# Optimization experiments

Measured on AMD Instinct MI355X. Metric: run time of the kernel, lower is better.

The kernel has to match this reference:

```python
import jax, jax.numpy as jnp
import numpy as np

B, S, D, H = 2, 2048, 1024, 16
DH = D // H
SCALE = 1.0 / np.sqrt(D).astype(np.float32)  # module uses sqrt(d_model), not sqrt(d_h)


def setup_inputs() -> dict:
    key = jax.random.key(0)
    ks = jax.random.split(key, 11)
    def lin(k):
        kw, kb = jax.random.split(k)
        W = jax.random.normal(kw, (D, D), jnp.float32) * 0.02
        b = jax.random.normal(kb, (D,), jnp.float32) * 0.02
        return W, b
    Wq, bq = lin(ks[0]); Wk, bk = lin(ks[1]); Wv, bv = lin(ks[2]); Wo, bo = lin(ks[3])
    Q = jax.random.normal(ks[4], (B, S, D), jnp.float32)
    K = jax.random.normal(ks[5], (B, S, D), jnp.float32)
    V = jax.random.normal(ks[6], (B, S, D), jnp.float32)
    mask = jnp.triu(jnp.ones((S, S), jnp.bool_), k=1)  # True = masked (causal)
    return {"Q": Q, "K": K, "V": V, "mask": mask,
            "Wq": Wq, "bq": bq, "Wk": Wk, "bk": bk,
            "Wv": Wv, "bv": bv, "Wo": Wo, "bo": bo}


def reference(Q, K, V, mask, Wq, bq, Wk, bk, Wv, bv, Wo, bo):
    # Linear projections (torch Linear: x @ W^T + b; W here stored pre-transposed)
    q = Q @ Wq + bq  # [B,S,D]
    k = K @ Wk + bk
    v = V @ Wv + bv
    # Faithful (scrambled) head split: transpose then reshape for Q and K
    qh = jnp.transpose(q, (0, 2, 1)).reshape(B, H, S, DH)
    kh = jnp.transpose(jnp.transpose(k, (0, 2, 1)).reshape(B, H, S, DH), (0, 1, 3, 2))  # [B,H,DH,S]
    score = jax.nn.softmax(jnp.matmul(qh, kh) * SCALE, axis=-1)  # [B,H,S,S]
    # Faithful post-softmax masking
    score = jnp.where(mask, jnp.float32(-1e9), score)
    # V is reshaped directly (no transpose) per the source
    att = jnp.matmul(score, v.reshape(B, H, S, DH))  # [B,H,S,DH]
    att = att.reshape(B, S, D)
    return att @ Wo + bo  # dropout is identity in eval
```

## Files before the change

### kernel.cpp

```cpp
#include <hip/hip_runtime.h>
#include <hip/hip_bf16.h>


typedef __hip_bfloat16 bf16;
typedef __attribute__((ext_vector_type(8))) short bf16x8;
typedef __attribute__((ext_vector_type(4))) float f32x4;
typedef __attribute__((address_space(1))) const unsigned int guint;
typedef __attribute__((address_space(3))) unsigned int luint;

constexpr size_t OFF_WCUMT  = 0;
constexpr size_t OFF_WBIGT  = 524288;
constexpr size_t OFF_VB     = 1572864;
constexpr size_t OFF_WVB    = 3670016;
constexpr size_t OFF_UBIG   = 4194304;
constexpr size_t OFF_WOSUMT = 8388608;
constexpr size_t OFF_WVFT   = 8454144;
constexpr size_t OFF_BBIG   = 8519680;
constexpr size_t OFF_BVF    = 8521728;
constexpr size_t OFF_FLAG   = 8521792;

__device__ __forceinline__ float toF(bf16 x)  { return __bfloat162float(x); }
__device__ __forceinline__ float toF(float x) { return x; }
__device__ __forceinline__ unsigned short f2b_bits(float f) {
    unsigned u = __float_as_uint(f);
    return (unsigned short)((u + 0x7FFF + ((u >> 16) & 1)) >> 16);
}

__global__ __launch_bounds__(256) void detect_dtype(const unsigned short* __restrict__ Vraw,
                                                    int* __restrict__ flag) {
    __shared__ int cnt[256];
    const int t = threadIdx.x;
    int weird = 0;
    #pragma unroll
    for (int j = 0; j < 8; ++j) {
        unsigned short h = Vraw[2 * (t * 8 + j)];
        int e = (h >> 7) & 0xFF;
        bool w = (e >= 127 + 21) || (e != 0 && e <= 127 - 21) ||
                 (e == 0 && (h & 0x7F));
        weird += w ? 1 : 0;
    }
    cnt[t] = weird;
    __syncthreads();
    #pragma unroll
    for (int s = 128; s > 0; s >>= 1) {
        if (t < s) cnt[t] += cnt[t + s];
        __syncthreads();
    }
    if (t == 0) *flag = (cnt[0] < 512) ? 1 : 0;
}

__global__ __launch_bounds__(256) void conv_f2b(const float* __restrict__ V,
                                                const float* __restrict__ Wv,
                                                bf16* __restrict__ Vb,
                                                bf16* __restrict__ Wvb,
                                                const int* __restrict__ flag) {
    if (*flag != 0) return;
    int i = blockIdx.x * 256 + threadIdx.x;
    float4 v;
    ushort4* dst;
    if (i < 1048576) {
        v = ((const float4*)V)[i];
        dst = ((ushort4*)Vb) + i;
    } else {
        int j = i - 1048576;
        if (j >= 262144) return;
        v = ((const float4*)Wv)[j];
        dst = ((ushort4*)Wvb) + j;
    }
    ushort4 h;
    h.x = f2b_bits(v.x); h.y = f2b_bits(v.y);
    h.z = f2b_bits(v.z); h.w = f2b_bits(v.w);
    *dst = h;
}

__global__ __launch_bounds__(256) void fold_weights(const void* __restrict__ WoR,
                                                    const void* __restrict__ WvR,
                                                    const void* __restrict__ bvR,
                                                    bf16* __restrict__ WcumT,
                                                    float* __restrict__ WoSumT,
                                                    float* __restrict__ WvFT,
                                                    float* __restrict__ bvF,
                                                    const int* __restrict__ flag) {
    const int f = *flag;
    int idx = blockIdx.x * 256 + threadIdx.x;
    int a = idx >> 6, dh = idx & 63;
    float acc = 0.f;
    if (f == 1) {
        const bf16* Wo = (const bf16*)WoR;
        #pragma unroll
        for (int q = 0; q < 16; ++q) {
            WcumT[(size_t)a * 1024 + q * 64 + dh] = __float2bfloat16(acc);
            acc += toF(Wo[(size_t)(q * 64 + dh) * 1024 + a]);
        }
    } else {
        const float* Wo = (const float*)WoR;
        #pragma unroll
        for (int q = 0; q < 16; ++q) {
            WcumT[(size_t)a * 1024 + q * 64 + dh] = __float2bfloat16(acc);
            acc += Wo[(size_t)(q * 64 + dh) * 1024 + a];
        }
    }
    WoSumT[(size_t)a * 64 + dh] = acc;
    float acc2 = 0.f;
    if (f == 1) {
        const bf16* Wv = (const bf16*)WvR;
        #pragma unroll
        for (int q = 0; q < 16; ++q)
            acc2 += toF(Wv[(size_t)a * 1024 + q * 64 + dh]);
    } else {
        const float* Wv = (const float*)WvR;
        #pragma unroll
        for (int q = 0; q < 16; ++q)
            acc2 += Wv[(size_t)a * 1024 + q * 64 + dh];
    }
    WvFT[(size_t)dh * 1024 + a] = acc2;
    if (idx < 64) {
        float b = 0.f;
        if (f == 1) {
            const bf16* bv = (const bf16*)bvR;
            #pragma unroll
            for (int q = 0; q < 16; ++q) b += toF(bv[q * 64 + idx]);
        } else {
            const float* bv = (const float*)bvR;
            #pragma unroll
            for (int q = 0; q < 16; ++q) b += ((const float*)bvR)[q * 64 + idx];
        }
        bvF[idx] = b;
    }
}

__global__ __launch_bounds__(64) void reduce_bias(const void* __restrict__ bvR,
                                                  const bf16* __restrict__ WcumT,
                                                  const float* __restrict__ WoSumT,
                                                  const float* __restrict__ bvF,
                                                  float* __restrict__ bbig,
                                                  const int* __restrict__ flag) {
    const int f = *flag;
    const int n = blockIdx.x, t = threadIdx.x;
    float acc = 0.f;
    if (n < 1024) {
        if (f == 1) {
            const bf16* bv = (const bf16*)bvR;
            for (int d = t; d < 1024; d += 64)
                acc += toF(bv[d]) * toF(WcumT[(size_t)n * 1024 + d]);
        } else {
            const float* bv = (const float*)bvR;
            for (int d = t; d < 1024; d += 64)
                acc += bv[d] * toF(WcumT[(size_t)n * 1024 + d]);
        }
    } else {
        acc = bvF[t] * WoSumT[(size_t)(n - 1024) * 64 + t];
    }
    #pragma unroll
    for (int off = 32; off > 0; off >>= 1) acc += __shfl_down(acc, off);
    if (t == 0) bbig[n] = acc;
}

__global__ __launch_bounds__(256, 2)
void gemm128w2(const float* __restrict__ A, int lda,
               const float* __restrict__ Bm, int ldb,
               bf16* __restrict__ C, int ldc, int K) {
    __shared__ __align__(16) float As[16][128];
    __shared__ __align__(16) float Bs[16][128];
    const int tid = threadIdx.x;
    const int tx = tid & 15, ty = tid >> 4;
    const int gx = gridDim.x;
    int lin = blockIdx.y * gx + blockIdx.x;
    const int nwg = gx * gridDim.y;
    if ((nwg & 7) == 0) { const int per = nwg >> 3; lin = (lin & 7) * per + (lin >> 3); }
    const int m0 = (lin / gx) * 128;
    const int n0 = (lin % gx) * 128;
    const int arow = tid >> 1, ahalf = (tid & 1) * 8;
    const int brow = tid >> 4, bcol = (tid & 15) * 4;
    float acc[8][8] = {};
    for (int k0 = 0; k0 < K; k0 += 16) {
        {
            const float* ap = A + (size_t)(m0 + arow) * lda + (k0 + ahalf);
            float4 a0 = *(const float4*)ap, a1 = *(const float4*)(ap + 4);
            As[ahalf + 0][arow] = a0.x; As[ahalf + 1][arow] = a0.y;
            As[ahalf + 2][arow] = a0.z; As[ahalf + 3][arow] = a0.w;
            As[ahalf + 4][arow] = a1.x; As[ahalf + 5][arow] = a1.y;
            As[ahalf + 6][arow] = a1.z; As[ahalf + 7][arow] = a1.w;
        }
        {
            const float* bp = Bm + (size_t)(k0 + brow) * ldb + n0 + bcol;
            float4 b0 = *(const float4*)bp;
            float4 b1 = *(const float4*)(bp + 64);
            *(float4*)&Bs[brow][bcol]      = b0;
            *(float4*)&Bs[brow][bcol + 64] = b1;
        }
        __syncthreads();
        #pragma unroll
        for (int kk = 0; kk < 16; ++kk) {
            float4 aL = *(const float4*)&As[kk][ty * 4];
            float4 aH = *(const float4*)&As[kk][64 + ty * 4];
            float4 bL = *(const float4*)&Bs[kk][tx * 4];
            float4 bH = *(const float4*)&Bs[kk][64 + tx * 4];
            float a[8] = {aL.x, aL.y, aL.z, aL.w, aH.x, aH.y, aH.z, aH.w};
            float b[8] = {bL.x, bL.y, bL.z, bL.w, bH.x, bH.y, bH.z, bH.w};
            #pragma unroll
            for (int i = 0; i < 8; ++i)
                #pragma unroll
                for (int j = 0; j < 8; ++j)
                    acc[i][j] += a[i] * b[j];
        }
        __syncthreads();
    }
    #pragma unroll
    for (int ih = 0; ih < 2; ++ih)
        #pragma unroll
        for (int ii = 0; ii < 4; ++ii) {
            const int m = m0 + ih * 64 + ty * 4 + ii;
            bf16* crow = C + (size_t)m * ldc + n0;
            #pragma unroll
            for (int jh = 0; jh < 2; ++jh)
                #pragma unroll
                for (int j = 0; j < 4; ++j)
                    crow[jh * 64 + tx * 4 + j] =
                        __float2bfloat16(acc[ih * 4 + ii][jh * 4 + j]);
        }
}

__global__ __launch_bounds__(256, 2)
void mfma_nt(const bf16* __restrict__ Abf, const bf16* __restrict__ Aalt,
             const bf16* __restrict__ Bbf, const bf16* __restrict__ Balt,
             int lda, int ldb,
             const float* __restrict__ bias,
             bf16* __restrict__ C, int ldc, int K,
             const int* __restrict__ flag) {
    const bf16* A  = (*flag == 1) ? Abf : Aalt;
    const bf16* BT = (*flag == 1) ? Bbf : Balt;
    __shared__ __align__(16) short AsS[8192];
    __shared__ __align__(16) short BsS[8192];

    const int tid  = threadIdx.x;
    const int lane = tid & 63;
    const int w    = tid >> 6;
    const int wr   = w >> 1, wc = w & 1;

    const int gx = gridDim.x;
    int lin = blockIdx.y * gx + blockIdx.x;
    const int nwg = gx * gridDim.y;
    if ((nwg & 7) == 0) { const int per = nwg >> 3; lin = (lin & 7) * per + (lin >> 3); }
    const int m0 = (lin / gx) * 128;
    const int n0 = (lin % gx) * 128;

    const int srow = lane >> 3;
    const int sk   = 8 * ((lane & 7) ^ srow);
    const bf16* Ag = A  + (size_t)(m0 + w * 32 + srow) * lda + sk;
    const bf16* Bg = BT + (size_t)(n0 + w * 32 + srow) * ldb + sk;
    char* AsB = (char*)AsS;
    char* BsB = (char*)BsS;

    const int row16 = lane & 15;
    const int arow  = (wr * 64 + row16) * 128;
    const int brow  = (wc * 64 + row16) * 128;
    const int kx    = (lane & 7) << 4;
    const int koff0 = (((lane >> 4) << 4)) ^ kx;
    const int koff1 = (64 | ((lane >> 4) << 4)) ^ kx;

    f32x4 acc[4][4];
    #pragma unroll
    for (int i = 0; i < 4; ++i)
        #pragma unroll
        for (int j = 0; j < 4; ++j)
            acc[i][j] = (f32x4){0.f, 0.f, 0.f, 0.f};

    for (int k0 = 0; k0 < K; k0 += 64) {
        #pragma unroll
        for (int q = 0; q < 4; ++q) {
            __builtin_amdgcn_global_load_lds((guint*)(Ag + k0 + (size_t)q * 8 * lda),
                                             (luint*)(AsB + w * 4096 + q * 1024),
                                             16, 0, 0);
            __builtin_amdgcn_global_load_lds((guint*)(Bg + k0 + (size_t)q * 8 * ldb),
                                             (luint*)(BsB + w * 4096 + q * 1024),
                                             16, 0, 0);
        }
        __syncthreads();
        #pragma unroll
        for (int ks = 0; ks < 2; ++ks) {
            const int ko = ks ? koff1 : koff0;
            bf16x8 af[4], bfv[4];
            #pragma unroll
            for (int i = 0; i < 4; ++i)
                af[i] = *(const bf16x8*)(AsB + arow + i * 2048 + ko);
            #pragma unroll
            for (int j = 0; j < 4; ++j)
                bfv[j] = *(const bf16x8*)(BsB + brow + j * 2048 + ko);
            #pragma unroll
            for (int i = 0; i < 4; ++i)
                #pragma unroll
                for (int j = 0; j < 4; ++j)
                    acc[i][j] = __builtin_amdgcn_mfma_f32_16x16x32_bf16(
                        af[i], bfv[j], acc[i][j], 0, 0, 0);
        }
        __syncthreads();
    }

    const int crow0 = (lane >> 4) * 4;
    float bb[4];
    #pragma unroll
    for (int j = 0; j < 4; ++j)
        bb[j] = bias ? bias[n0 + wc * 64 + j * 16 + row16] : 0.f;
    #pragma unroll
    for (int i = 0; i < 4; ++i) {
        #pragma unroll
        for (int r = 0; r < 4; ++r) {
            const int m = m0 + wr * 64 + i * 16 + crow0 + r;
            bf16* cp = C + (size_t)m * ldc + n0 + wc * 64 + row16;
            #pragma unroll
            for (int j = 0; j < 4; ++j)
                cp[j * 16] = __float2bfloat16(acc[i][j][r] + bb[j]);
        }
    }
}

__global__ __launch_bounds__(256) void scan_all(const bf16* __restrict__ ubig,
                                                const void* __restrict__ boR,
                                                void* __restrict__ outR,
                                                const int* __restrict__ flag) {
    const int f = *flag;
    const int n = blockIdx.x * 256 + threadIdx.x;
    const int h = blockIdx.y, b = blockIdx.z;
    const size_t rowbase = (size_t)b * 2048 + (size_t)h * 128;
    if (f == 1) {
        const float bias = toF(((const bf16*)boR)[n]);
        bf16* out = (bf16*)outR;
        float acc = 0.f;
        #pragma unroll 4
        for (int t = 127; t >= 0; --t) {
            const size_t row = rowbase + t;
            const float uval = toF(ubig[row * 2048 + n]);
            const float gval = toF(ubig[row * 2048 + 1024 + n]);
            out[row * 1024 + n] = __float2bfloat16(bias - 1e9f * (acc + uval));
            acc += gval;
        }
    } else {
        const float bias = ((const float*)boR)[n];
        float* out = (float*)outR;
        float acc = 0.f;
        #pragma unroll 4
        for (int t = 127; t >= 0; --t) {
            const size_t row = rowbase + t;
            const float uval = toF(ubig[row * 2048 + n]);
            const float gval = toF(ubig[row * 2048 + 1024 + n]);
            out[row * 1024 + n] = bias - 1e9f * (acc + uval);
            acc += gval;
        }
    }
}


extern "C" void kernel_launch(void* const* d_in, const int* in_sizes, int n_in,
                              void* d_out, int out_size, void* d_ws, size_t ws_size,
                              hipStream_t stream) {
    float* ws = (float*)d_ws;
    int* flag = (int*)(ws + OFF_FLAG);

    bf16*  WcumT  = (bf16*)(ws + OFF_WCUMT);
    bf16*  WbigT  = (bf16*)(ws + OFF_WBIGT);
    bf16*  Vb     = (bf16*)(ws + OFF_VB);
    bf16*  Wvb    = (bf16*)(ws + OFF_WVB);
    bf16*  ubig   = (bf16*)(ws + OFF_UBIG);
    float* WoSumT = ws + OFF_WOSUMT;
    float* WvFT   = ws + OFF_WVFT;
    float* bbig   = ws + OFF_BBIG;
    float* bvF    = ws + OFF_BVF;

    detect_dtype<<<1, 256, 0, stream>>>((const unsigned short*)d_in[2], flag);
    conv_f2b<<<5120, 256, 0, stream>>>((const float*)d_in[2], (const float*)d_in[8],
                                       Vb, Wvb, flag);
    fold_weights<<<256, 256, 0, stream>>>(d_in[10], d_in[8], d_in[9],
                                          WcumT, WoSumT, WvFT, bvF, flag);
    reduce_bias<<<2048, 64, 0, stream>>>(d_in[9], WcumT, WoSumT, bvF, bbig, flag);
    gemm128w2<<<dim3(8, 8), 256, 0, stream>>>(WoSumT, 64, WvFT, 1024,
                                              WbigT + (size_t)1024 * 1024, 1024, 64);
    mfma_nt<<<dim3(8, 8), 256, 0, stream>>>(WcumT, WcumT,
                                            (const bf16*)d_in[8], Wvb,
                                            1024, 1024, nullptr,
                                            WbigT, 1024, 1024, flag);
    mfma_nt<<<dim3(16, 32), 256, 0, stream>>>((const bf16*)d_in[2], Vb,
                                              WbigT, WbigT,
                                              1024, 1024, bbig,
                                              ubig, 2048, 1024, flag);
    scan_all<<<dim3(4, 16, 2), 256, 0, stream>>>(ubig, d_in[11], d_out, flag);
}
```

Baseline: 204.8 us.

## Move causal suffix-scan onto V input and fuse output epilogue into GEMM

Instead of computing a wide GEMM producing a 2048-column intermediate and then scanning it along rows, the scan is moved onto the input V (suffix sums computed by a new kernel), and the main GEMM concatenates [V | Vsuffix] along K against [WvcT; W2T], writing the final output directly with bias and -1e9 scaling in the epilogue. The GEMM kernel becomes 512-thread, double-buffered LDS with 128x128 tiles split across 8 waves. This removes the large ubig intermediate write/read and the separate scan kernel, at the cost of a serial 128-step suffix kernel over V and a doubled K dimension.

```diff
diff --git a/kernel.cpp b/kernel.cpp
--- a/kernel.cpp
+++ b/kernel.cpp
@@ -9,18 +9,18 @@
 typedef __attribute__((address_space(3))) unsigned int luint;
 
 constexpr size_t OFF_WCUMT  = 0;
-constexpr size_t OFF_WBIGT  = 524288;
+constexpr size_t OFF_WVCT   = 524288;
+constexpr size_t OFF_W2T    = 1048576;
 constexpr size_t OFF_VB     = 1572864;
-constexpr size_t OFF_WVB    = 3670016;
-constexpr size_t OFF_UBIG   = 4194304;
-constexpr size_t OFF_WOSUMT = 8388608;
-constexpr size_t OFF_WVFT   = 8454144;
-constexpr size_t OFF_BBIG   = 8519680;
-constexpr size_t OFF_BVF    = 8521728;
-constexpr size_t OFF_FLAG   = 8521792;
+constexpr size_t OFF_VSUFB  = 3670016;
+constexpr size_t OFF_WVB    = 5767168;
+constexpr size_t OFF_WOSUMT = 6291456;
+constexpr size_t OFF_WVFT   = 6356992;
+constexpr size_t OFF_BBIG   = 6422528;
+constexpr size_t OFF_BVF    = 6424576;
+constexpr size_t OFF_FLAG   = 6424640;
 
 __device__ __forceinline__ float toF(bf16 x)  { return __bfloat162float(x); }
-__device__ __forceinline__ float toF(float x) { return x; }
 __device__ __forceinline__ unsigned short f2b_bits(float f) {
     unsigned u = __float_as_uint(f);
     return (unsigned short)((u + 0x7FFF + ((u >> 16) & 1)) >> 16);
@@ -49,28 +49,39 @@
     if (t == 0) *flag = (cnt[0] < 512) ? 1 : 0;
 }
 
-__global__ __launch_bounds__(256) void conv_f2b(const float* __restrict__ V,
-                                                const float* __restrict__ Wv,
-                                                bf16* __restrict__ Vb,
-                                                bf16* __restrict__ Wvb,
-                                                const int* __restrict__ flag) {
+__global__ __launch_bounds__(256) void vsuffix(const void* __restrict__ VR,
+                                               bf16* __restrict__ Vb,
+                                               bf16* __restrict__ Vsufb,
+                                               const int* __restrict__ flag) {
+    const int f = *flag;
+    const int n = blockIdx.x * 256 + threadIdx.x;
+    const int h = blockIdx.y, b = blockIdx.z;
+    const size_t rowbase = (size_t)b * 2048 + (size_t)h * 128;
+    float acc = 0.f;
+    for (int t = 127; t >= 0; --t) {
+        const size_t row = rowbase + t;
+        float v;
+        if (f == 1) {
+            v = toF(((const bf16*)VR)[row * 1024 + n]);
+        } else {
+            v = ((const float*)VR)[row * 1024 + n];
+            Vb[row * 1024 + n] = __float2bfloat16(v);
+        }
+        Vsufb[row * 1024 + n] = __float2bfloat16(acc);
+        acc += v;
+    }
+}
+
+__global__ __launch_bounds__(256) void conv_wv(const float* __restrict__ Wv,
+                                               bf16* __restrict__ Wvb,
+                                               const int* __restrict__ flag) {
     if (*flag != 0) return;
     int i = blockIdx.x * 256 + threadIdx.x;
-    float4 v;
-    ushort4* dst;
-    if (i < 1048576) {
-        v = ((const float4*)V)[i];
-        dst = ((ushort4*)Vb) + i;
-    } else {
-        int j = i - 1048576;
-        if (j >= 262144) return;
-        v = ((const float4*)Wv)[j];
-        dst = ((ushort4*)Wvb) + j;
-    }
+    float4 v = ((const float4*)Wv)[i];
     ushort4 h;
     h.x = f2b_bits(v.x); h.y = f2b_bits(v.y);
     h.z = f2b_bits(v.z); h.w = f2b_bits(v.w);
-    *dst = h;
+    ((ushort4*)Wvb)[i] = h;
 }
 
 __global__ __launch_bounds__(256) void fold_weights(const void* __restrict__ WoR,
@@ -121,7 +132,6 @@
             #pragma unroll
             for (int q = 0; q < 16; ++q) b += toF(bv[q * 64 + idx]);
         } else {
-            const float* bv = (const float*)bvR;
             #pragma unroll
             for (int q = 0; q < 16; ++q) b += ((const float*)bvR)[q * 64 + idx];
         }
@@ -221,132 +231,138 @@
         }
 }
 
-__global__ __launch_bounds__(256, 2)
-void mfma_nt(const bf16* __restrict__ Abf, const bf16* __restrict__ Aalt,
-             const bf16* __restrict__ Bbf, const bf16* __restrict__ Balt,
-             int lda, int ldb,
-             const float* __restrict__ bias,
-             bf16* __restrict__ C, int ldc, int K,
-             const int* __restrict__ flag) {
-    const bf16* A  = (*flag == 1) ? Abf : Aalt;
-    const bf16* BT = (*flag == 1) ? Bbf : Balt;
-    __shared__ __align__(16) short AsS[8192];
-    __shared__ __align__(16) short BsS[8192];
+template <int FUSED>
+__global__ __launch_bounds__(512, 2)
+void mfma8(const bf16* __restrict__ A0, const bf16* __restrict__ A0a,
+           const bf16* __restrict__ A1,
+           const bf16* __restrict__ B0, const bf16* __restrict__ B0a,
+           const bf16* __restrict__ B1,
+           int ksplit, int K,
+           const float* __restrict__ bbig, const void* __restrict__ boR,
+           void* __restrict__ Cout, int ldc,
+           const int* __restrict__ flag) {
+    const int fl = *flag;
+    const bf16* A0s = (fl == 1) ? A0 : A0a;
+    const bf16* B0s = (fl == 1) ? B0 : B0a;
+    __shared__ __align__(16) char ldsb[65536];
 
     const int tid  = threadIdx.x;
     const int lane = tid & 63;
-    const int w    = tid >> 6;
-    const int wr   = w >> 1, wc = w & 1;
+    const int wv   = tid >> 6;
+    const int wr   = wv >> 2, wc = wv & 3;
 
     const int gx = gridDim.x;
     int lin = blockIdx.y * gx + blockIdx.x;
     const int nwg = gx * gridDim.y;
-    if ((nwg & 7) == 0) { const int per = nwg >> 3; lin = (lin & 7) * per + (lin >> 3); }
+    { const int per = nwg >> 3; lin = (lin & 7) * per + (lin >> 3); }
     const int m0 = (lin / gx) * 128;
     const int n0 = (lin % gx) * 128;
 
-    const int srow = lane >> 3;
-    const int sk   = 8 * ((lane & 7) ^ srow);
-    const bf16* Ag = A  + (size_t)(m0 + w * 32 + srow) * lda + sk;
-    const bf16* Bg = BT + (size_t)(n0 + w * 32 + srow) * ldb + sk;
-    char* AsB = (char*)AsS;
-    char* BsB = (char*)BsS;
+    const int c0row = tid >> 3;
+    const int c0k   = 8 * ((tid & 7) ^ (c0row & 7));
+    const int c1row = c0row + 64;
+    const int c1k   = 8 * ((tid & 7) ^ (c1row & 7));
+    const int wb0   = wv * 1024;
+    const int wb1   = 8192 + wv * 1024;
+
+    auto stage = [&](int t, int d) {
+        const int kb = t << 6;
+        const bf16 *As_, *Bs_; int ka;
+        if (kb < ksplit) { As_ = A0s; Bs_ = B0s; ka = kb; }
+        else             { As_ = A1;  Bs_ = B1;  ka = kb - ksplit; }
+        const int db = d * 32768;
+        __builtin_amdgcn_global_load_lds((guint*)(As_ + (size_t)(m0 + c0row) * 1024 + ka + c0k),
+                                         (luint*)(ldsb + db + wb0), 16, 0, 0);
+        __builtin_amdgcn_global_load_lds((guint*)(Bs_ + (size_t)(n0 + c0row) * 1024 + ka + c0k),
+                                         (luint*)(ldsb + db + 16384 + wb0), 16, 0, 0);
+        __builtin_amdgcn_global_load_lds((guint*)(As_ + (size_t)(m0 + c1row) * 1024 + ka + c1k),
+                                         (luint*)(ldsb + db + wb1), 16, 0, 0);
+        __builtin_amdgcn_global_load_lds((guint*)(Bs_ + (size_t)(n0 + c1row) * 1024 + ka + c1k),
+                                         (luint*)(ldsb + db + 16384 + wb1), 16, 0, 0);
+    };
 
     const int row16 = lane & 15;
     const int arow  = (wr * 64 + row16) * 128;
-    const int brow  = (wc * 64 + row16) * 128;
+    const int brow  = (wc * 32 + row16) * 128;
     const int kx    = (lane & 7) << 4;
     const int koff0 = (((lane >> 4) << 4)) ^ kx;
     const int koff1 = (64 | ((lane >> 4) << 4)) ^ kx;
 
-    f32x4 acc[4][4];
+    f32x4 acc[4][2];
     #pragma unroll
     for (int i = 0; i < 4; ++i)
         #pragma unroll
-        for (int j = 0; j < 4; ++j)
+        for (int j = 0; j < 2; ++j)
             acc[i][j] = (f32x4){0.f, 0.f, 0.f, 0.f};
 
-    for (int k0 = 0; k0 < K; k0 += 64) {
-        #pragma unroll
-        for (int q = 0; q < 4; ++q) {
-            __builtin_amdgcn_global_load_lds((guint*)(Ag + k0 + (size_t)q * 8 * lda),
-                                             (luint*)(AsB + w * 4096 + q * 1024),
-                                             16, 0, 0);
-            __builtin_amdgcn_global_load_lds((guint*)(Bg + k0 + (size_t)q * 8 * ldb),
-                                             (luint*)(BsB + w * 4096 + q * 1024),
-                                             16, 0, 0);
-        }
-        __syncthreads();
+    const int nt = K >> 6;
+    stage(0, 0);
+    __syncthreads();
+    int cur = 0;
+    for (int t = 0; t < nt; ++t) {
+        if (t + 1 < nt) stage(t + 1, cur ^ 1);
+        const char* Ab = ldsb + cur * 32768;
+        const char* Bb = Ab + 16384;
         #pragma unroll
         for (int ks = 0; ks < 2; ++ks) {
             const int ko = ks ? koff1 : koff0;
-            bf16x8 af[4], bfv[4];
+            bf16x8 af[4], bf2[2];
             #pragma unroll
             for (int i = 0; i < 4; ++i)
-                af[i] = *(const bf16x8*)(AsB + arow + i * 2048 + ko);
-            #pragma unroll
-            for (int j = 0; j < 4; ++j)
-                bfv[j] = *(const bf16x8*)(BsB + brow + j * 2048 + ko);
+                af[i] = *(const bf16x8*)(Ab + arow + i * 2048 + ko);
+            #pragma unroll
+            for (int j = 0; j < 2; ++j)
+                bf2[j] = *(const bf16x8*)(Bb + brow + j * 2048 + ko);
             #pragma unroll
             for (int i = 0; i < 4; ++i)
                 #pragma unroll
-                for (int j = 0; j < 4; ++j)
+                for (int j = 0; j < 2; ++j)
                     acc[i][j] = __builtin_amdgcn_mfma_f32_16x16x32_bf16(
-                        af[i], bfv[j], acc[i][j], 0, 0, 0);
+                        af[i], bf2[j], acc[i][j], 0, 0, 0);
         }
         __syncthreads();
+        cur ^= 1;
     }
 
     const int crow0 = (lane >> 4) * 4;
-    float bb[4];
-    #pragma unroll
-    for (int j = 0; j < 4; ++j)
-        bb[j] = bias ? bias[n0 + wc * 64 + j * 16 + row16] : 0.f;
-    #pragma unroll
-    for (int i = 0; i < 4; ++i) {
-        #pragma unroll
-        for (int r = 0; r < 4; ++r) {
-            const int m = m0 + wr * 64 + i * 16 + crow0 + r;
-            bf16* cp = C + (size_t)m * ldc + n0 + wc * 64 + row16;
-            #pragma unroll
-            for (int j = 0; j < 4; ++j)
-                cp[j * 16] = __float2bfloat16(acc[i][j][r] + bb[j]);
-        }
-    }
-}
-
-__global__ __launch_bounds__(256) void scan_all(const bf16* __restrict__ ubig,
-                                                const void* __restrict__ boR,
-                                                void* __restrict__ outR,
-                                                const int* __restrict__ flag) {
-    const int f = *flag;
-    const int n = blockIdx.x * 256 + threadIdx.x;
-    const int h = blockIdx.y, b = blockIdx.z;
-    const size_t rowbase = (size_t)b * 2048 + (size_t)h * 128;
-    if (f == 1) {
-        const float bias = toF(((const bf16*)boR)[n]);
-        bf16* out = (bf16*)outR;
-        float acc = 0.f;
-        #pragma unroll 4
-        for (int t = 127; t >= 0; --t) {
-            const size_t row = rowbase + t;
-            const float uval = toF(ubig[row * 2048 + n]);
-            const float gval = toF(ubig[row * 2048 + 1024 + n]);
-            out[row * 1024 + n] = __float2bfloat16(bias - 1e9f * (acc + uval));
-            acc += gval;
-        }
+    if (FUSED) {
+        float bo_[2], bvc_[2], b2_[2];
+        int nn[2];
+        #pragma unroll
+        for (int j = 0; j < 2; ++j) {
+            const int n = n0 + wc * 32 + j * 16 + row16;
+            nn[j]   = n;
+            bo_[j]  = (fl == 1) ? toF(((const bf16*)boR)[n]) : ((const float*)boR)[n];
+            bvc_[j] = bbig[n];
+            b2_[j]  = bbig[1024 + n];
+        }
+        #pragma unroll
+        for (int i = 0; i < 4; ++i)
+            #pragma unroll
+            for (int r = 0; r < 4; ++r) {
+                const int m = m0 + wr * 64 + i * 16 + crow0 + r;
+                const float wsuf = (float)(127 - (m & 127));
+                #pragma unroll
+                for (int j = 0; j < 2; ++j) {
+                    const float res = bo_[j] -
+                        1e9f * (acc[i][j][r] + bvc_[j] + wsuf * b2_[j]);
+                    if (fl == 1)
+                        ((bf16*)Cout)[(size_t)m * 1024 + nn[j]] = __float2bfloat16(res);
+                    else
+                        ((float*)Cout)[(size_t)m * 1024 + nn[j]] = res;
+                }
+            }
     } else {
-        const float bias = ((const float*)boR)[n];
-        float* out = (float*)outR;
-        float acc = 0.f;
-        #pragma unroll 4
-        for (int t = 127; t >= 0; --t) {
-            const size_t row = rowbase + t;
-            const float uval = toF(ubig[row * 2048 + n]);
-            const float gval = toF(ubig[row * 2048 + 1024 + n]);
-            out[row * 1024 + n] = bias - 1e9f * (acc + uval);
-            acc += gval;
-        }
+        #pragma unroll
+        for (int i = 0; i < 4; ++i)
+            #pragma unroll
+            for (int r = 0; r < 4; ++r) {
+                const int m = m0 + wr * 64 + i * 16 + crow0 + r;
+                bf16* cp = (bf16*)Cout + (size_t)m * ldc + n0 + wc * 32 + row16;
+                #pragma unroll
+                for (int j = 0; j < 2; ++j)
+                    cp[j * 16] = __float2bfloat16(acc[i][j][r]);
+            }
     }
 }
 
@@ -358,30 +374,30 @@
     int* flag = (int*)(ws + OFF_FLAG);
 
     bf16*  WcumT  = (bf16*)(ws + OFF_WCUMT);
-    bf16*  WbigT  = (bf16*)(ws + OFF_WBIGT);
+    bf16*  WvcT   = (bf16*)(ws + OFF_WVCT);
+    bf16*  W2T    = (bf16*)(ws + OFF_W2T);
     bf16*  Vb     = (bf16*)(ws + OFF_VB);
+    bf16*  Vsufb  = (bf16*)(ws + OFF_VSUFB);
     bf16*  Wvb    = (bf16*)(ws + OFF_WVB);
-    bf16*  ubig   = (bf16*)(ws + OFF_UBIG);
     float* WoSumT = ws + OFF_WOSUMT;
     float* WvFT   = ws + OFF_WVFT;
     float* bbig   = ws + OFF_BBIG;
     float* bvF    = ws + OFF_BVF;
 
     detect_dtype<<<1, 256, 0, stream>>>((const unsigned short*)d_in[2], flag);
-    conv_f2b<<<5120, 256, 0, stream>>>((const float*)d_in[2], (const float*)d_in[8],
-                                       Vb, Wvb, flag);
+    vsuffix<<<dim3(4, 16, 2), 256, 0, stream>>>(d_in[2], Vb, Vsufb, flag);
+    conv_wv<<<1024, 256, 0, stream>>>((const float*)d_in[8], Wvb, flag);
     fold_weights<<<256, 256, 0, stream>>>(d_in[10], d_in[8], d_in[9],
                                           WcumT, WoSumT, WvFT, bvF, flag);
     reduce_bias<<<2048, 64, 0, stream>>>(d_in[9], WcumT, WoSumT, bvF, bbig, flag);
     gemm128w2<<<dim3(8, 8), 256, 0, stream>>>(WoSumT, 64, WvFT, 1024,
-                                              WbigT + (size_t)1024 * 1024, 1024, 64);
-    mfma_nt<<<dim3(8, 8), 256, 0, stream>>>(WcumT, WcumT,
-                                            (const bf16*)d_in[8], Wvb,
-                                            1024, 1024, nullptr,
-                                            WbigT, 1024, 1024, flag);
-    mfma_nt<<<dim3(16, 32), 256, 0, stream>>>((const bf16*)d_in[2], Vb,
-                                              WbigT, WbigT,
-                                              1024, 1024, bbig,
-                                              ubig, 2048, 1024, flag);
-    scan_all<<<dim3(4, 16, 2), 256, 0, stream>>>(ubig, d_in[11], d_out, flag);
-}
+                                              W2T, 1024, 64);
+    mfma8<0><<<dim3(8, 8), 512, 0, stream>>>(WcumT, WcumT, WcumT,
+                                             (const bf16*)d_in[8], Wvb, Wvb,
+                                             1024, 1024, nullptr, nullptr,
+                                             WvcT, 1024, flag);
+    mfma8<1><<<dim3(8, 32), 512, 0, stream>>>((const bf16*)d_in[2], Vb, Vsufb,
+                                              WvcT, WvcT, W2T,
+                                              1024, 2048, bbig, d_in[11],
+                                              d_out, 1024, flag);
+}
```

After: 248.4 us. 21.3% more time.
